# Kernel tuning notes

Hardware: AMD Instinct MI355X
Metric: run time of the kernel (lower is better)

## Reference

```python
import jax, jax.numpy as jnp
import numpy as np

B, T = 2, 1024
D_MODEL = 2048
D_STATE = 64            # N
HEADDIM = 64            # P (module sets headdim = d_state)
EXPAND = 2
D_CONV = 4
NGROUPS = 1
D_INNER = EXPAND * D_MODEL                     # 4096
NHEADS = D_INNER // HEADDIM                    # 64
CONV_DIM = D_INNER + 2 * NGROUPS * D_STATE     # 4224
D_IN_PROJ = 2 * D_INNER + 2 * NGROUPS * D_STATE + NHEADS  # 8384
EPS = 1e-5


def setup_inputs() -> dict:
    key = jax.random.key(0)
    k = jax.random.split(key, 10)
    n = lambda kk, sh, sc: jax.random.normal(kk, sh, jnp.float32) * sc
    return {
        "x": n(k[0], (B, T, D_MODEL), 1.0),
        "ln_w": jnp.ones((D_MODEL,), jnp.float32),
        "ln_b": jnp.zeros((D_MODEL,), jnp.float32),
        "in_proj_w": n(k[1], (D_IN_PROJ, D_MODEL), D_MODEL ** -0.5),
        "conv_w": n(k[2], (CONV_DIM, D_CONV), 0.5),
        "conv_b": n(k[3], (CONV_DIM,), 0.02),
        "dt_bias": n(k[4], (NHEADS,), 0.5),
        "A_log": jnp.log(jax.random.uniform(k[5], (NHEADS,), jnp.float32, 1.0, 16.0)),
        "D": 1.0 + n(k[6], (NHEADS,), 0.1),
        "norm_w": jnp.ones((D_INNER,), jnp.float32),
        "out_proj_w": n(k[7], (D_MODEL, D_INNER), D_INNER ** -0.5),
    }


def _layernorm(x, w, b):
    mu = x.mean(-1, keepdims=True)
    var = ((x - mu) ** 2).mean(-1, keepdims=True)
    return (x - mu) * jax.lax.rsqrt(var + EPS) * w + b


def _mamba2(u, in_proj_w, conv_w, conv_b, dt_bias, A_log, D, norm_w, out_proj_w):
    zxbcdt = u @ in_proj_w.T                         # [B,T,D_IN_PROJ]
    z = zxbcdt[..., :D_INNER]                        # gate
    xBC = zxbcdt[..., D_INNER:D_INNER + CONV_DIM]
    dt = zxbcdt[..., D_INNER + CONV_DIM:]            # [B,T,H]
    # causal depthwise conv1d (kernel size D_CONV) + SiLU
    xp = jnp.pad(xBC, ((0, 0), (D_CONV - 1, 0), (0, 0)))
    conv = conv_b
    for kk in range(D_CONV):
        conv = conv + xp[:, kk:kk + T, :] * conv_w[:, kk]
    xBC = jax.nn.silu(conv)
    x_in = xBC[..., :D_INNER].reshape(B, T, NHEADS, HEADDIM)   # [B,T,H,P]
    Bm = xBC[..., D_INNER:D_INNER + D_STATE]         # [B,T,N] (ngroups=1)
    Cm = xBC[..., D_INNER + D_STATE:]                # [B,T,N]
    dt = jax.nn.softplus(dt + dt_bias)               # [B,T,H]
    A = -jnp.exp(A_log)                              # [H]
    dA = jnp.exp(dt * A)                             # [B,T,H]
    dtx = dt[..., None] * x_in                       # [B,T,H,P]

    def step(h, inp):
        dA_t, dtx_t, B_t, C_t = inp
        # h: [B,H,P,N]
        h = h * dA_t[:, :, None, None] + dtx_t[..., None] * B_t[:, None, None, :]
        y = jnp.einsum('bhpn,bn->bhp', h, C_t)
        return h, y

    h0 = jnp.zeros((B, NHEADS, HEADDIM, D_STATE), u.dtype)
    xs = (jnp.moveaxis(dA, 1, 0), jnp.moveaxis(dtx, 1, 0),
          jnp.moveaxis(Bm, 1, 0), jnp.moveaxis(Cm, 1, 0))
    _, ys = jax.lax.scan(step, h0, xs)               # ys: [T,B,H,P]
    y = jnp.moveaxis(ys, 0, 1) + D[:, None] * x_in   # skip term D*x
    y = y.reshape(B, T, D_INNER)
    # gated RMSNorm (norm_before_gate=False): rmsnorm(y * silu(z)) * w
    y = y * jax.nn.silu(z)
    y = y * jax.lax.rsqrt((y * y).mean(-1, keepdims=True) + EPS) * norm_w
    return y @ out_proj_w.T                          # [B,T,D_MODEL]


def reference(x, ln_w, ln_b, in_proj_w, conv_w, conv_b, dt_bias, A_log, D, norm_w, out_proj_w):
    # pre-norm Mamba2 block with residual: x + Mamba2(LayerNorm(x))
    return x + _mamba2(_layernorm(x, ln_w, ln_b), in_proj_w, conv_w, conv_b,
                       dt_bias, A_log, D, norm_w, out_proj_w)
```

## Files before the change

kernel.cpp:

```cpp
#include <hip/hip_runtime.h>
#include <hip/hip_bf16.h>

#define Bdim 2
#define Tdim 1024
#define DMODEL 2048
#define DSTATE 64
#define HEADDIM 64
#define DCONV 4
#define DINNER 4096
#define NHEADS 64
#define CONVDIM 4224
#define DINPROJ 8384
#define NPAD 8448
#define MROWS (Bdim*Tdim)
#define QC 64
#define NCHUNK (Tdim/QC)

typedef __attribute__((ext_vector_type(8))) short bf16x8;
typedef __attribute__((ext_vector_type(4))) float f32x4;
typedef __attribute__((ext_vector_type(4))) unsigned short u16x4;
typedef __attribute__((ext_vector_type(8))) unsigned short u16x8;

#define GLB(p) ((const __attribute__((address_space(1))) void*)(p))
#define LDS(p) ((__attribute__((address_space(3))) void*)(p))

__device__ __forceinline__ unsigned short f2bf(float f) {
    unsigned int x = __builtin_bit_cast(unsigned int, f);
    x += 0x7fffu + ((x >> 16) & 1u);
    return (unsigned short)(x >> 16);
}
__device__ __forceinline__ float bf2f(unsigned int u16) {
    unsigned int x = u16 << 16;
    return __builtin_bit_cast(float, x);
}
__device__ __forceinline__ float siluf(float v) {
    return v / (1.f + expf(-v));
}

#define CVT_A4 (NPAD * DMODEL / 4)
#define CVT_B4 (DMODEL * DINNER / 4)
#define CVT_BLKS ((CVT_A4 + CVT_B4) / 256)
__global__ __launch_bounds__(256) void prep_k(const float* __restrict__ in_proj,
                                              const float* __restrict__ out_proj,
                                              unsigned short* __restrict__ win,
                                              unsigned short* __restrict__ wout,
                                              const float* __restrict__ x,
                                              const float* __restrict__ lw,
                                              const float* __restrict__ lb,
                                              unsigned short* __restrict__ u) {
    if (blockIdx.x < CVT_BLKS) {
        int idx = blockIdx.x * 256 + threadIdx.x;
        if (idx < CVT_A4) {
            int i4 = idx * 4;
            int row = i4 >> 11;
            u16x4 o;
            if (row < DINPROJ) {
                float4 v = *(const float4*)(in_proj + i4);
                o = (u16x4){f2bf(v.x), f2bf(v.y), f2bf(v.z), f2bf(v.w)};
            } else {
                o = (u16x4){0, 0, 0, 0};
            }
            *(u16x4*)(win + i4) = o;
        } else {
            int i4 = (idx - CVT_A4) * 4;
            float4 v = *(const float4*)(out_proj + i4);
            *(u16x4*)(wout + i4) = (u16x4){f2bf(v.x), f2bf(v.y), f2bf(v.z), f2bf(v.w)};
        }
        return;
    }
    int row = blockIdx.x - CVT_BLKS;
    const float* xr = x + (size_t)row * DMODEL;
    float4 v[2];
    float s = 0.f, s2 = 0.f;
#pragma unroll
    for (int i = 0; i < 2; ++i) {
        int c = (threadIdx.x + 256 * i) * 4;
        v[i] = *(const float4*)(xr + c);
        s += v[i].x + v[i].y + v[i].z + v[i].w;
        s2 += v[i].x * v[i].x + v[i].y * v[i].y + v[i].z * v[i].z + v[i].w * v[i].w;
    }
#pragma unroll
    for (int off = 32; off; off >>= 1) { s += __shfl_down(s, off); s2 += __shfl_down(s2, off); }
    __shared__ float rs[4], rs2[4];
    if ((threadIdx.x & 63) == 0) { rs[threadIdx.x >> 6] = s; rs2[threadIdx.x >> 6] = s2; }
    __syncthreads();
    s = rs[0] + rs[1] + rs[2] + rs[3];
    s2 = rs2[0] + rs2[1] + rs2[2] + rs2[3];
    float mu = s * (1.f / DMODEL);
    float var = s2 * (1.f / DMODEL) - mu * mu;
    float inv = rsqrtf(var + 1e-5f);
#pragma unroll
    for (int i = 0; i < 2; ++i) {
        int c = (threadIdx.x + 256 * i) * 4;
        float4 wv = *(const float4*)(lw + c);
        float4 bv = *(const float4*)(lb + c);
        u16x4 o = {f2bf((v[i].x - mu) * inv * wv.x + bv.x),
                   f2bf((v[i].y - mu) * inv * wv.y + bv.y),
                   f2bf((v[i].z - mu) * inv * wv.z + bv.z),
                   f2bf((v[i].w - mu) * inv * wv.w + bv.w)};
        *(u16x4*)(u + (size_t)row * DMODEL + c) = o;
    }
}

#define WAITV(n) asm volatile("s_waitcnt vmcnt(" #n ")" ::: "memory")
#define LGKM0   do { asm volatile("s_waitcnt lgkmcnt(0)" ::: "memory"); \
                     __builtin_amdgcn_sched_barrier(0); } while (0)
#define SCB     __builtin_amdgcn_sched_barrier(0)
#define BAR     __builtin_amdgcn_s_barrier()

template <int EPI, int BM, int BN, int KTILES>
__global__ __launch_bounds__(512, 4) void gemm_cr(const unsigned short* __restrict__ A,
                                                  const unsigned short* __restrict__ Bw,
                                                  float* __restrict__ Cout,
                                                  const float* __restrict__ resid,
                                                  int N, int lda, int ldb,
                                                  int nb, int mb) {
    constexpr int NA = BM / 64;
    constexpr int NB = BN / 64;
    constexpr int IM = BM / 64;
    constexpr int IMH = IM / 2;
    constexpr int IN = BN / 32;

    __shared__ unsigned short As[2][BM * 64];
    __shared__ unsigned short Bs[2][BN * 64];

    const int bid = blockIdx.x;
    const int per_panel = mb * 8;
    const int fullp = (nb / 8) * per_panel;
    int mt, nt;
    if (bid < fullp) {
        int p = bid / per_panel, r = bid % per_panel;
        nt = p * 8 + r / mb; mt = r % mb;
    } else {
        int r = bid - fullp;
        nt = (nb / 8) * 8 + r / mb; mt = r % mb;
    }
    const int m0 = mt * BM, n0 = nt * BN;

    const int tid = threadIdx.x;
    const int lane = tid & 63, w = tid >> 6;
    const int wm = (w >> 1) * (BM / 4);
    const int wn = (w & 1) * (BN / 2);
    const int row16 = lane & 15, quad = lane >> 4;
    const int swz = row16 & 7;

    const unsigned short* gA[NA];
    const unsigned short* gB[NB];
#pragma unroll
    for (int l = 0; l < NA; ++l) {
        int c = l * 512 + tid, r = c >> 3, kb = (c & 7) ^ (r & 7);
        gA[l] = A + (size_t)(m0 + r) * lda + kb * 8;
    }
#pragma unroll
    for (int l = 0; l < NB; ++l) {
        int c = l * 512 + tid, r = c >> 3, kb = (c & 7) ^ (r & 7);
        gB[l] = Bw + (size_t)(n0 + r) * ldb + kb * 8;
    }

#define STG_A(d, kt) do { _Pragma("unroll")                                           \
    for (int _l = 0; _l < NA; ++_l)                                                   \
        __builtin_amdgcn_global_load_lds(GLB(gA[_l] + (kt) * 64),                     \
                LDS(&As[d][(_l * 512 + tid) * 8]), 16, 0, 0); } while (0)
#define STG_B(d, kt) do { _Pragma("unroll")                                           \
    for (int _l = 0; _l < NB; ++_l)                                                   \
        __builtin_amdgcn_global_load_lds(GLB(gB[_l] + (kt) * 64),                     \
                LDS(&Bs[d][(_l * 512 + tid) * 8]), 16, 0, 0); } while (0)
#define WAITN() do { if constexpr (NA == 2) WAITV(2); else WAITV(4); } while (0)
#define RD_B(d) do { _Pragma("unroll") for (int _j = 0; _j < IN; ++_j)                \
                     _Pragma("unroll") for (int _kc = 0; _kc < 2; ++_kc) {            \
                         int _row = wn + _j * 16 + row16;                             \
                         int _g = (_kc * 4 + quad) ^ swz;                             \
                         bfr[_j][_kc] = *(const bf16x8*)&Bs[d][(_row * 8 + _g) * 8];  \
                     } } while (0)
#define RD_A(d, h) do { _Pragma("unroll") for (int _i = 0; _i < IMH; ++_i)            \
                        _Pragma("unroll") for (int _kc = 0; _kc < 2; ++_kc) {         \
                            int _row = wm + ((h) * IMH + _i) * 16 + row16;            \
                            int _g = (_kc * 4 + quad) ^ swz;                          \
                            af[_i][_kc] = *(const bf16x8*)&As[d][(_row * 8 + _g) * 8];\
                        } } while (0)
#define MM(h) do { __builtin_amdgcn_s_setprio(1);                                     \
                   _Pragma("unroll") for (int _kc = 0; _kc < 2; ++_kc)                \
                   _Pragma("unroll") for (int _i = 0; _i < IMH; ++_i)                 \
                   _Pragma("unroll") for (int _j = 0; _j < IN; ++_j)                  \
                       acc[(h) * IMH + _i][_j] = __builtin_amdgcn_mfma_f32_16x16x32_bf16( \
                           af[_i][_kc], bfr[_j][_kc], acc[(h) * IMH + _i][_j], 0, 0, 0);  \
                   __builtin_amdgcn_s_setprio(0); } while (0)

    f32x4 acc[IM][IN];
#pragma unroll
    for (int i = 0; i < IM; ++i)
#pragma unroll
        for (int j = 0; j < IN; ++j) acc[i][j] = (f32x4){0.f, 0.f, 0.f, 0.f};
    bf16x8 bfr[IN][2], af[IMH][2];

    STG_A(0, 0); STG_B(0, 0);

    const int KI = KTILES / 2;
    for (int i = 0; i < KI; ++i) {
        const int k1 = 2 * i + 1, k2 = 2 * i + 2;
        const bool st2 = (k2 < KTILES);
        STG_A(1, k1);
        WAITN();
        BAR;
        RD_B(0); RD_A(0, 0);
        LGKM0;
        MM(0);
        BAR;
        RD_A(0, 1);
        STG_B(1, k1);
        BAR;
        LGKM0;
        MM(1);
        BAR;
        if (st2) {
            STG_A(0, k2);
            WAITN();
        } else {
            WAITV(0);
        }
        BAR;
        RD_B(1); RD_A(1, 0);
        LGKM0;
        MM(0);
        BAR;
        RD_A(1, 1);
        if (st2) STG_B(0, k2);
        BAR;
        LGKM0;
        MM(1);
        BAR;
    }

#pragma unroll
    for (int i = 0; i < IM; ++i)
#pragma unroll
        for (int j = 0; j < IN; ++j)
#pragma unroll
            for (int r = 0; r < 4; ++r) {
                int m = m0 + wm + i * 16 + quad * 4 + r;
                int n = n0 + wn + j * 16 + row16;
                float v = acc[i][j][r];
                if (EPI == 0)
                    Cout[(size_t)m * N + n] = v;
                else
                    Cout[(size_t)m * N + n] = resid[(size_t)m * N + n] + v;
            }
#undef STG_A
#undef STG_B
#undef WAITN
#undef RD_A
#undef RD_B
#undef MM
}

#define CONV_T (MROWS * CONVDIM / 4)
__global__ __launch_bounds__(256) void convdt_k(const float* __restrict__ zx,
                                                const float* __restrict__ cw,
                                                const float* __restrict__ cb,
                                                const float* __restrict__ dt_bias,
                                                const float* __restrict__ A_log,
                                                float* __restrict__ xin,
                                                float* __restrict__ bcf,
                                                float* __restrict__ dtf,
                                                float* __restrict__ dtAf) {
    int idx = blockIdx.x * 256 + threadIdx.x;
    if (idx < CONV_T) {
        int cg = idx % (CONVDIM / 4);
        int bt = idx / (CONVDIM / 4);
        int c = cg * 4;
        int t = bt & (Tdim - 1);
        const float* base = zx + (size_t)bt * NPAD + DINNER + c;
        float4 acc = *(const float4*)(cb + c);
#pragma unroll
        for (int kk = 0; kk < DCONV; ++kk) {
            int tt = t - 3 + kk;
            if (tt >= 0) {
                float4 v = *(const float4*)(base + (long)(kk - 3) * NPAD);
                acc.x += v.x * cw[(c + 0) * 4 + kk];
                acc.y += v.y * cw[(c + 1) * 4 + kk];
                acc.z += v.z * cw[(c + 2) * 4 + kk];
                acc.w += v.w * cw[(c + 3) * 4 + kk];
            }
        }
        float4 s = {siluf(acc.x), siluf(acc.y), siluf(acc.z), siluf(acc.w)};
        if (c < DINNER) *(float4*)(xin + (size_t)bt * DINNER + c) = s;
        else            *(float4*)(bcf + (size_t)bt * 128 + (c - DINNER)) = s;
    } else {
        int d4 = (idx - CONV_T) * 4;
        int bt = d4 >> 6;
        int h = d4 & 63;
        float4 raw = *(const float4*)(zx + (size_t)bt * NPAD + (DINNER + CONVDIM) + h);
        float4 bias = *(const float4*)(dt_bias + h);
        float4 al = *(const float4*)(A_log + h);
        float r[4] = {raw.x + bias.x, raw.y + bias.y, raw.z + bias.z, raw.w + bias.w};
        float A[4] = {-expf(al.x), -expf(al.y), -expf(al.z), -expf(al.w)};
        float4 dtv, dta;
        float* dtp = (float*)&dtv; float* dap = (float*)&dta;
#pragma unroll
        for (int j = 0; j < 4; ++j) {
            float dv = (r[j] > 20.f) ? r[j] : log1pf(expf(r[j]));
            dtp[j] = dv;
            dap[j] = dv * A[j];
        }
        *(float4*)(dtf + bt * 64 + h) = dtv;
        *(float4*)(dtAf + bt * 64 + h) = dta;
    }
}

__global__ __launch_bounds__(256) void chunk_state_k(const float* __restrict__ xin,
                                                     const float* __restrict__ bcf,
                                                     const float* __restrict__ dtf,
                                                     const float* __restrict__ dtAf,
                                                     float* __restrict__ Sst,
                                                     float* __restrict__ laq) {
    const int blk = blockIdx.x;
    const int c = blk & 15, h = (blk >> 4) & 63, b = blk >> 10;
    const int bt0 = b * Tdim + c * QC;
    const int tid = threadIdx.x;

    __shared__ float Bs[QC][68];
    __shared__ float Dx[QC][68];
    __shared__ float wsh[QC];

    if (tid < QC) {
        float v = dtAf[(bt0 + tid) * NHEADS + h];
#pragma unroll
        for (int d = 1; d < 64; d <<= 1) {
            float o = __shfl_up(v, d, 64);
            v += (tid >= d) ? o : 0.f;
        }
        float la63 = __shfl(v, 63, 64);
        wsh[tid] = expf(la63 - v);
        if (tid == 63) laq[blk] = la63;
    }
    __syncthreads();

    const int row = tid >> 2, q = tid & 3;
    {
        float m = wsh[row] * dtf[(bt0 + row) * NHEADS + h];
        const float* xr = xin + (size_t)(bt0 + row) * DINNER + h * 64 + q * 16;
        const float* br = bcf + (size_t)(bt0 + row) * 128 + q * 16;
#pragma unroll
        for (int j = 0; j < 4; ++j) {
            float4 xv = *(const float4*)(xr + j * 4);
            float4 bv = *(const float4*)(br + j * 4);
            *(float4*)&Dx[row][q * 16 + j * 4] = (float4){m * xv.x, m * xv.y, m * xv.z, m * xv.w};
            *(float4*)&Bs[row][q * 16 + j * 4] = bv;
        }
    }
    __syncthreads();

    const int p0 = (tid >> 4) * 4, n0 = (tid & 15) * 4;
    float acc[4][4] = {};
    for (int i = 0; i < QC; ++i) {
        float4 dv = *(const float4*)&Dx[i][p0];
        float4 bv = *(const float4*)&Bs[i][n0];
        float dva[4] = {dv.x, dv.y, dv.z, dv.w};
        float bva[4] = {bv.x, bv.y, bv.z, bv.w};
#pragma unroll
        for (int a = 0; a < 4; ++a)
#pragma unroll
            for (int e = 0; e < 4; ++e) acc[a][e] += dva[a] * bva[e];
    }
    float* Sp = Sst + (size_t)blk * NPAD;
#pragma unroll
    for (int a = 0; a < 4; ++a)
        *(float4*)&Sp[(p0 + a) * 64 + n0] = (float4){acc[a][0], acc[a][1], acc[a][2], acc[a][3]};
}

__global__ __launch_bounds__(256) void combine_k(float* __restrict__ Sst,
                                                 const float* __restrict__ laq) {
    const int bh = blockIdx.x >> 1;
    const int half = blockIdx.x & 1;
    const int tid = threadIdx.x;
    float4 r0 = {}, r1 = {};
    for (int c = 0; c < NCHUNK - 1; ++c) {
        float* p = Sst + (size_t)(bh * 16 + c) * NPAD + half * 2048 + tid * 8;
        float P = expf(laq[bh * 16 + c]);
        float4 s0 = ((const float4*)p)[0], s1 = ((const float4*)p)[1];
        r0 = (float4){P * r0.x + s0.x, P * r0.y + s0.y, P * r0.z + s0.z, P * r0.w + s0.w};
        r1 = (float4){P * r1.x + s1.x, P * r1.y + s1.y, P * r1.z + s1.z, P * r1.w + s1.w};
        ((float4*)p)[0] = r0; ((float4*)p)[1] = r1;
    }
}

__global__ __launch_bounds__(256) void chunk_out_k2(float* __restrict__ xin,
                                                    const float* __restrict__ bcf,
                                                    const float* __restrict__ dtf,
                                                    const float* __restrict__ dtAf,
                                                    const float* __restrict__ Sst,
                                                    const float* __restrict__ Dp) {
    const int blk = blockIdx.x;
    const int c = blk & 15, h = (blk >> 4) & 63, b = blk >> 10;
    const int bt0 = b * Tdim + c * QC;
    const int tid = threadIdx.x;

    __shared__ unsigned short Csh[64 * 64];
    __shared__ unsigned short Bsh[64 * 64];
    __shared__ unsigned short DxT[64 * 64];
    __shared__ unsigned short Gh [64 * 64];
    __shared__ unsigned short Hh [64 * 64];
    __shared__ float lash[QC];

    if (tid < QC) {
        float v = dtAf[(bt0 + tid) * NHEADS + h];
#pragma unroll
        for (int d = 1; d < 64; d <<= 1) {
            float o = __shfl_up(v, d, 64);
            v += (tid >= d) ? o : 0.f;
        }
        lash[tid] = v;
    }

    const int row = tid >> 2, q = tid & 3;
    {
        float m = dtf[(bt0 + row) * NHEADS + h];
        const float* xr = xin + (size_t)(bt0 + row) * DINNER + h * 64 + q * 16;
        const float* br = bcf + (size_t)(bt0 + row) * 128 + q * 16;
        const float* cr = bcf + (size_t)(bt0 + row) * 128 + 64 + q * 16;
        float xb[16];
        u16x8 cc[2], bb[2];
#pragma unroll
        for (int j = 0; j < 4; ++j) {
            float4 xv = *(const float4*)(xr + j * 4);
            float4 bv = *(const float4*)(br + j * 4);
            float4 cv = *(const float4*)(cr + j * 4);
            xb[j * 4 + 0] = m * xv.x; xb[j * 4 + 1] = m * xv.y;
            xb[j * 4 + 2] = m * xv.z; xb[j * 4 + 3] = m * xv.w;
            int hi = j >> 1, lo = (j & 1) * 4;
            cc[hi][lo + 0] = f2bf(cv.x); cc[hi][lo + 1] = f2bf(cv.y);
            cc[hi][lo + 2] = f2bf(cv.z); cc[hi][lo + 3] = f2bf(cv.w);
            bb[hi][lo + 0] = f2bf(bv.x); bb[hi][lo + 1] = f2bf(bv.y);
            bb[hi][lo + 2] = f2bf(bv.z); bb[hi][lo + 3] = f2bf(bv.w);
        }
        const int base = row * 64;
        const int c0 = ((q * 2) ^ (row & 7)) * 8, c1 = ((q * 2 + 1) ^ (row & 7)) * 8;
        *(u16x8*)&Csh[base + c0] = cc[0];  *(u16x8*)&Csh[base + c1] = cc[1];
        *(u16x8*)&Bsh[base + c0] = bb[0];  *(u16x8*)&Bsh[base + c1] = bb[1];
#pragma unroll
        for (int k2 = 0; k2 < 16; ++k2) {
            int p = q * 16 + k2;
            DxT[p * 64 + (((row >> 3) ^ (p & 7)) * 8 + (row & 7))] = f2bf(xb[k2]);
        }
        if (c > 0) {
            const float* Hp = Sst + (size_t)(blk - 1) * NPAD + row * 64 + q * 16;
            u16x8 hh[2];
#pragma unroll
            for (int j = 0; j < 4; ++j) {
                float4 hv = *(const float4*)(Hp + j * 4);
                int hi = j >> 1, lo = (j & 1) * 4;
                hh[hi][lo + 0] = f2bf(hv.x); hh[hi][lo + 1] = f2bf(hv.y);
                hh[hi][lo + 2] = f2bf(hv.z); hh[hi][lo + 3] = f2bf(hv.w);
            }
            *(u16x8*)&Hh[base + c0] = hh[0];  *(u16x8*)&Hh[base + c1] = hh[1];
        }
    }
    __syncthreads();

    const int lane = tid & 63, w = tid >> 6;
    const int t0 = w * 16;
    const int row16 = lane & 15, quad = lane >> 4;
    const int swz = row16 & 7;

    f32x4 a1[4];
#pragma unroll
    for (int st = 0; st < 4; ++st) a1[st] = (f32x4){0.f, 0.f, 0.f, 0.f};
#pragma unroll
    for (int kc = 0; kc < 2; ++kc) {
        int g = ((kc * 4 + quad) ^ swz) * 8;
        bf16x8 ca = *(const bf16x8*)&Csh[(t0 + row16) * 64 + g];
#pragma unroll
        for (int st = 0; st < 4; ++st) {
            bf16x8 bs = *(const bf16x8*)&Bsh[(st * 16 + row16) * 64 + g];
            a1[st] = __builtin_amdgcn_mfma_f32_16x16x32_bf16(ca, bs, a1[st], 0, 0, 0);
        }
    }
    float latv[4];
#pragma unroll
    for (int r = 0; r < 4; ++r) latv[r] = lash[t0 + quad * 4 + r];
#pragma unroll
    for (int st = 0; st < 4; ++st) {
        int s = st * 16 + row16;
        float las = lash[s];
#pragma unroll
        for (int r = 0; r < 4; ++r) {
            int t = t0 + quad * 4 + r;
            float gv = (s <= t) ? a1[st][r] * expf(latv[r] - las) : 0.f;
            Gh[t * 64 + (((s >> 3) ^ (t & 7)) * 8 + (s & 7))] = f2bf(gv);
        }
    }
    __syncthreads();

    f32x4 aS[4], aH[4];
#pragma unroll
    for (int pt = 0; pt < 4; ++pt) { aS[pt] = (f32x4){0.f,0.f,0.f,0.f}; aH[pt] = (f32x4){0.f,0.f,0.f,0.f}; }
#pragma unroll
    for (int kc = 0; kc < 2; ++kc) {
        int g = ((kc * 4 + quad) ^ swz) * 8;
        bf16x8 ga = *(const bf16x8*)&Gh[(t0 + row16) * 64 + g];
#pragma unroll
        for (int pt = 0; pt < 4; ++pt) {
            bf16x8 db = *(const bf16x8*)&DxT[(pt * 16 + row16) * 64 + g];
            aS[pt] = __builtin_amdgcn_mfma_f32_16x16x32_bf16(ga, db, aS[pt], 0, 0, 0);
        }
        if (c > 0) {
            bf16x8 ca = *(const bf16x8*)&Csh[(t0 + row16) * 64 + g];
#pragma unroll
            for (int pt = 0; pt < 4; ++pt) {
                bf16x8 hb = *(const bf16x8*)&Hh[(pt * 16 + row16) * 64 + g];
                aH[pt] = __builtin_amdgcn_mfma_f32_16x16x32_bf16(ca, hb, aH[pt], 0, 0, 0);
            }
        }
    }

    float Dh = Dp[h];
    float eA[4];
#pragma unroll
    for (int r = 0; r < 4; ++r) eA[r] = expf(latv[r]);
#pragma unroll
    for (int pt = 0; pt < 4; ++pt)
#pragma unroll
        for (int r = 0; r < 4; ++r) {
            int t = t0 + quad * 4 + r, p = pt * 16 + row16;
            float* xr2 = xin + (size_t)(bt0 + t) * DINNER + h * 64 + p;
            float xv = *xr2;
            float y = aS[pt][r] + Dh * xv;
            if (c > 0) y += eA[r] * aH[pt][r];
            *xr2 = y;
        }
}

__global__ __launch_bounds__(256) void gate_k(const float* __restrict__ ybf,
                                              const float* __restrict__ zx,
                                              const float* __restrict__ nw,
                                              unsigned short* __restrict__ yg,
                                              int ldyg) {
    int row = blockIdx.x;
    float4 tv[4];
    float s2 = 0.f;
#pragma unroll
    for (int i = 0; i < 4; ++i) {
        int c = (threadIdx.x + 256 * i) * 4;
        float4 y = *(const float4*)(ybf + (size_t)row * DINNER + c);
        float4 z = *(const float4*)(zx + (size_t)row * NPAD + c);
        float4 t = {y.x * siluf(z.x), y.y * siluf(z.y), y.z * siluf(z.z), y.w * siluf(z.w)};
        tv[i] = t;
        s2 += t.x * t.x + t.y * t.y + t.z * t.z + t.w * t.w;
    }
#pragma unroll
    for (int off = 32; off; off >>= 1) s2 += __shfl_down(s2, off);
    __shared__ float rs[4];
    if ((threadIdx.x & 63) == 0) rs[threadIdx.x >> 6] = s2;
    __syncthreads();
    s2 = rs[0] + rs[1] + rs[2] + rs[3];
    float scale = rsqrtf(s2 * (1.f / DINNER) + 1e-5f);
#pragma unroll
    for (int i = 0; i < 4; ++i) {
        int c = (threadIdx.x + 256 * i) * 4;
        float4 w = *(const float4*)(nw + c);
        u16x4 o = {f2bf(tv[i].x * scale * w.x), f2bf(tv[i].y * scale * w.y),
                   f2bf(tv[i].z * scale * w.z), f2bf(tv[i].w * scale * w.w)};
        *(u16x4*)(yg + (size_t)row * ldyg + c) = o;
    }
}

extern "C" void kernel_launch(void* const* d_in, const int* in_sizes, int n_in,
                              void* d_out, int out_size, void* d_ws, size_t ws_size,
                              hipStream_t stream) {
    const float* x        = (const float*)d_in[0];
    const float* ln_w     = (const float*)d_in[1];
    const float* ln_b     = (const float*)d_in[2];
    const float* in_proj  = (const float*)d_in[3];
    const float* conv_w   = (const float*)d_in[4];
    const float* conv_b   = (const float*)d_in[5];
    const float* dt_bias  = (const float*)d_in[6];
    const float* A_log    = (const float*)d_in[7];
    const float* Dp       = (const float*)d_in[8];
    const float* norm_w   = (const float*)d_in[9];
    const float* out_proj = (const float*)d_in[10];
    float* out = (float*)d_out;
    char* ws = (char*)d_ws;

    float*          zx   = (float*)(ws + 0);
    unsigned short* wout = (unsigned short*)(ws + 69206016);
    unsigned short* win  = (unsigned short*)(ws + 85983232);
    unsigned short* ubf  = (unsigned short*)(ws + 120586240);
    float*          xin  = (float*)(ws + 85983232);
    float*          bcf  = (float*)(ws + 120586240);
    float*          dtf  = (float*)(ws + 121634816);
    float*          dtAf = (float*)(ws + 122159104);
    float*          laq  = (float*)(ws + 122683392);
    float*          Sst  = zx + 4096;
    unsigned short* yg   = (unsigned short*)zx + 8192;
    const int       ldyg = 16896;

    prep_k<<<CVT_BLKS + MROWS, 256, 0, stream>>>(in_proj, out_proj, win, wout,
                                                 x, ln_w, ln_b, ubf);
    gemm_cr<0, 128, 128, 32><<<66 * 16, 512, 0, stream>>>(ubf, win, zx, nullptr,
                                                          NPAD, DMODEL, DMODEL, 66, 16);
    convdt_k<<<(CONV_T + MROWS * NHEADS / 4) / 256, 256, 0, stream>>>(zx, conv_w, conv_b,
                                                                      dt_bias, A_log,
                                                                      xin, bcf, dtf, dtAf);
    chunk_state_k<<<Bdim * NHEADS * NCHUNK, 256, 0, stream>>>(xin, bcf, dtf, dtAf, Sst, laq);
    combine_k<<<2 * Bdim * NHEADS, 256, 0, stream>>>(Sst, laq);
    chunk_out_k2<<<Bdim * NHEADS * NCHUNK, 256, 0, stream>>>(xin, bcf, dtf, dtAf, Sst, Dp);
    gate_k<<<MROWS, 256, 0, stream>>>(xin, zx, norm_w, yg, ldyg);
    gemm_cr<1, 128, 64, 64><<<32 * 16, 512, 0, stream>>>(yg, wout, out, x,
                                                         DMODEL, ldyg, DINNER, 32, 16);
}
```

Before: 428.1 us.

## Add dedicated 256x128 K32 in-proj GEMM and retune out-proj GEMM thread count

Replaces the in-projection GEMM with a new kernel that uses 256x128 tiles and 32-wide K steps. It has a repacked, swizzled LDS layout, a simpler double-buffered loop and a 4x4 MFMA block per wave. The out-projection GEMM is generalised over thread count and launched with 256 threads, so each wave covers more rows. The aim is more reuse per loaded tile and less scheduling overhead, at the cost of fewer blocks and more barriers per K step.

```diff
diff --git a/kernel.cpp b/kernel.cpp
--- a/kernel.cpp
+++ b/kernel.cpp
@@ -108,21 +108,15 @@
 #define SCB     __builtin_amdgcn_sched_barrier(0)
 #define BAR     __builtin_amdgcn_s_barrier()
 
-template <int EPI, int BM, int BN, int KTILES>
-__global__ __launch_bounds__(512, 4) void gemm_cr(const unsigned short* __restrict__ A,
-                                                  const unsigned short* __restrict__ Bw,
-                                                  float* __restrict__ Cout,
-                                                  const float* __restrict__ resid,
-                                                  int N, int lda, int ldb,
-                                                  int nb, int mb) {
-    constexpr int NA = BM / 64;
-    constexpr int NB = BN / 64;
-    constexpr int IM = BM / 64;
-    constexpr int IMH = IM / 2;
-    constexpr int IN = BN / 32;
-
-    __shared__ unsigned short As[2][BM * 64];
-    __shared__ unsigned short Bs[2][BN * 64];
+template <int KTILES>
+__global__ __launch_bounds__(512, 4) void gemm1_k32(const unsigned short* __restrict__ A,
+                                                    const unsigned short* __restrict__ Bw,
+                                                    float* __restrict__ Cout,
+                                                    int N, int lda, int ldb,
+                                                    int nb, int mb) {
+    constexpr int BM = 256, BN = 128;
+    __shared__ unsigned short As[2][BM * 32];
+    __shared__ unsigned short Bs[2][BN * 32];
 
     const int bid = blockIdx.x;
     const int per_panel = mb * 8;
@@ -139,7 +133,126 @@
 
     const int tid = threadIdx.x;
     const int lane = tid & 63, w = tid >> 6;
-    const int wm = (w >> 1) * (BM / 4);
+    const int wm = (w >> 1) * 64;
+    const int wn = (w & 1) * 64;
+    const int row16 = lane & 15, quad = lane >> 4;
+
+    const unsigned short* gA[2];
+    const unsigned short* gB0;
+#pragma unroll
+    for (int l = 0; l < 2; ++l) {
+        int c = l * 512 + tid, rp = c >> 3, gp = (c & 7) ^ (rp & 7);
+        int row = rp * 2 + (gp >> 2), kb = gp & 3;
+        gA[l] = A + (size_t)(m0 + row) * lda + kb * 8;
+    }
+    {
+        int c = tid, rp = c >> 3, gp = (c & 7) ^ (rp & 7);
+        int row = rp * 2 + (gp >> 2), kb = gp & 3;
+        gB0 = Bw + (size_t)(n0 + row) * ldb + kb * 8;
+    }
+
+    int aoff[4], boff[4];
+#pragma unroll
+    for (int i = 0; i < 4; ++i) {
+        int row = wm + i * 16 + row16, rp = row >> 1;
+        int s = (((row & 1) << 2) + quad) ^ (rp & 7);
+        aoff[i] = rp * 64 + s * 8;
+    }
+#pragma unroll
+    for (int j = 0; j < 4; ++j) {
+        int row = wn + j * 16 + row16, rp = row >> 1;
+        int s = (((row & 1) << 2) + quad) ^ (rp & 7);
+        boff[j] = rp * 64 + s * 8;
+    }
+
+#define STG(d, kt) do {                                                            \
+    __builtin_amdgcn_global_load_lds(GLB(gA[0] + (kt) * 32),                       \
+                                     LDS(&As[d][tid * 8]), 16, 0, 0);              \
+    __builtin_amdgcn_global_load_lds(GLB(gA[1] + (kt) * 32),                       \
+                                     LDS(&As[d][(512 + tid) * 8]), 16, 0, 0);      \
+    __builtin_amdgcn_global_load_lds(GLB(gB0 + (kt) * 32),                         \
+                                     LDS(&Bs[d][tid * 8]), 16, 0, 0);              \
+} while (0)
+
+    f32x4 acc[4][4];
+#pragma unroll
+    for (int i = 0; i < 4; ++i)
+#pragma unroll
+        for (int j = 0; j < 4; ++j) acc[i][j] = (f32x4){0.f, 0.f, 0.f, 0.f};
+    bf16x8 bfr[4], af[4];
+
+    STG(0, 0);
+    int cur = 0;
+    for (int t = 0; t < KTILES; ++t) {
+        if (t + 1 < KTILES) {
+            STG(cur ^ 1, t + 1);
+            WAITV(3);
+        } else {
+            WAITV(0);
+        }
+        BAR;
+#pragma unroll
+        for (int j = 0; j < 4; ++j) bfr[j] = *(const bf16x8*)&Bs[cur][boff[j]];
+#pragma unroll
+        for (int i = 0; i < 4; ++i) af[i] = *(const bf16x8*)&As[cur][aoff[i]];
+        LGKM0;
+        __builtin_amdgcn_s_setprio(1);
+#pragma unroll
+        for (int i = 0; i < 4; ++i)
+#pragma unroll
+            for (int j = 0; j < 4; ++j)
+                acc[i][j] = __builtin_amdgcn_mfma_f32_16x16x32_bf16(af[i], bfr[j], acc[i][j], 0, 0, 0);
+        __builtin_amdgcn_s_setprio(0);
+        BAR;
+        cur ^= 1;
+    }
+
+#pragma unroll
+    for (int i = 0; i < 4; ++i)
+#pragma unroll
+        for (int j = 0; j < 4; ++j)
+#pragma unroll
+            for (int r = 0; r < 4; ++r) {
+                int m = m0 + wm + i * 16 + quad * 4 + r;
+                int n = n0 + wn + j * 16 + row16;
+                Cout[(size_t)m * N + n] = acc[i][j][r];
+            }
+#undef STG
+}
+
+template <int EPI, int NT, int BM, int BN, int KTILES>
+__global__ __launch_bounds__(NT, 4) void gemm_cr(const unsigned short* __restrict__ A,
+                                                 const unsigned short* __restrict__ Bw,
+                                                 float* __restrict__ Cout,
+                                                 const float* __restrict__ resid,
+                                                 int N, int lda, int ldb,
+                                                 int nb, int mb) {
+    constexpr int MW = NT / 128;
+    constexpr int NA = BM * 64 / 8 / NT;
+    constexpr int NB = BN * 64 / 8 / NT;
+    constexpr int IM = BM / MW / 16;
+    constexpr int IMH = IM / 2;
+    constexpr int IN = BN / 2 / 16;
+
+    __shared__ unsigned short As[2][BM * 64];
+    __shared__ unsigned short Bs[2][BN * 64];
+
+    const int bid = blockIdx.x;
+    const int per_panel = mb * 8;
+    const int fullp = (nb / 8) * per_panel;
+    int mt, nt;
+    if (bid < fullp) {
+        int p = bid / per_panel, r = bid % per_panel;
+        nt = p * 8 + r / mb; mt = r % mb;
+    } else {
+        int r = bid - fullp;
+        nt = (nb / 8) * 8 + r / mb; mt = r % mb;
+    }
+    const int m0 = mt * BM, n0 = nt * BN;
+
+    const int tid = threadIdx.x;
+    const int lane = tid & 63, w = tid >> 6;
+    const int wm = (w >> 1) * (BM / MW);
     const int wn = (w & 1) * (BN / 2);
     const int row16 = lane & 15, quad = lane >> 4;
     const int swz = row16 & 7;
@@ -148,23 +261,23 @@
     const unsigned short* gB[NB];
 #pragma unroll
     for (int l = 0; l < NA; ++l) {
-        int c = l * 512 + tid, r = c >> 3, kb = (c & 7) ^ (r & 7);
+        int c = l * NT + tid, r = c >> 3, kb = (c & 7) ^ (r & 7);
         gA[l] = A + (size_t)(m0 + r) * lda + kb * 8;
     }
 #pragma unroll
     for (int l = 0; l < NB; ++l) {
-        int c = l * 512 + tid, r = c >> 3, kb = (c & 7) ^ (r & 7);
+        int c = l * NT + tid, r = c >> 3, kb = (c & 7) ^ (r & 7);
         gB[l] = Bw + (size_t)(n0 + r) * ldb + kb * 8;
     }
 
 #define STG_A(d, kt) do { _Pragma("unroll")                                           \
     for (int _l = 0; _l < NA; ++_l)                                                   \
         __builtin_amdgcn_global_load_lds(GLB(gA[_l] + (kt) * 64),                     \
-                LDS(&As[d][(_l * 512 + tid) * 8]), 16, 0, 0); } while (0)
+                LDS(&As[d][(_l * NT + tid) * 8]), 16, 0, 0); } while (0)
 #define STG_B(d, kt) do { _Pragma("unroll")                                           \
     for (int _l = 0; _l < NB; ++_l)                                                   \
         __builtin_amdgcn_global_load_lds(GLB(gB[_l] + (kt) * 64),                     \
-                LDS(&Bs[d][(_l * 512 + tid) * 8]), 16, 0, 0); } while (0)
+                LDS(&Bs[d][(_l * NT + tid) * 8]), 16, 0, 0); } while (0)
 #define WAITN() do { if constexpr (NA == 2) WAITV(2); else WAITV(4); } while (0)
 #define RD_B(d) do { _Pragma("unroll") for (int _j = 0; _j < IN; ++_j)                \
                      _Pragma("unroll") for (int _kc = 0; _kc < 2; ++_kc) {            \
@@ -596,8 +709,7 @@
 
     prep_k<<<CVT_BLKS + MROWS, 256, 0, stream>>>(in_proj, out_proj, win, wout,
                                                  x, ln_w, ln_b, ubf);
-    gemm_cr<0, 128, 128, 32><<<66 * 16, 512, 0, stream>>>(ubf, win, zx, nullptr,
-                                                          NPAD, DMODEL, DMODEL, 66, 16);
+    gemm1_k32<64><<<66 * 8, 512, 0, stream>>>(ubf, win, zx, NPAD, DMODEL, DMODEL, 66, 8);
     convdt_k<<<(CONV_T + MROWS * NHEADS / 4) / 256, 256, 0, stream>>>(zx, conv_w, conv_b,
                                                                       dt_bias, A_log,
                                                                       xin, bcf, dtf, dtAf);
@@ -605,6 +717,6 @@
     combine_k<<<2 * Bdim * NHEADS, 256, 0, stream>>>(Sst, laq);
     chunk_out_k2<<<Bdim * NHEADS * NCHUNK, 256, 0, stream>>>(xin, bcf, dtf, dtAf, Sst, Dp);
     gate_k<<<MROWS, 256, 0, stream>>>(xin, zx, norm_w, yg, ldyg);
-    gemm_cr<1, 128, 64, 64><<<32 * 16, 512, 0, stream>>>(yg, wout, out, x,
-                                                         DMODEL, ldyg, DINNER, 32, 16);
-}
+    gemm_cr<1, 256, 128, 64, 64><<<32 * 16, 256, 0, stream>>>(yg, wout, out, x,
+                                                              DMODEL, ldyg, DINNER, 32, 16);
+}
```

After: 463.6 us. 1.08x slower.
